# Kernel tuning notes

Measured on AMD Instinct MI355X. Metric: run time of the kernel, lower is better.

Reference implementation:

```python
import jax, jax.numpy as jnp
import numpy as np


def setup_inputs() -> dict:
    key = jax.random.key(0)
    ks = jax.random.split(key, 8)
    B, S, H, E = 4, 4096, 768, 64
    hidden_states = jax.random.normal(ks[0], (B, S, H), dtype=jnp.float32)
    attention_mask = jnp.ones((B, S), dtype=jnp.float32)
    entity_positions = jax.random.randint(ks[1], (B, E), 0, S)
    scale = 1.0 / np.sqrt(H)
    Wq = jax.random.normal(ks[2], (H, H), dtype=jnp.float32) * scale
    bq = jnp.zeros((H,), dtype=jnp.float32)
    Wk = jax.random.normal(ks[3], (H, H), dtype=jnp.float32) * scale
    bk = jnp.zeros((H,), dtype=jnp.float32)
    Wv = jax.random.normal(ks[4], (H, H), dtype=jnp.float32) * scale
    bv = jnp.zeros((H,), dtype=jnp.float32)
    return {"hidden_states": hidden_states, "attention_mask": attention_mask,
            "entity_positions": entity_positions,
            "Wq": Wq, "bq": bq, "Wk": Wk, "bk": bk, "Wv": Wv, "bv": bv}


def reference(hidden_states, attention_mask, entity_positions, Wq, bq, Wk, bk, Wv, bv):
    B, S, H = hidden_states.shape
    scaling = jnp.sqrt(jnp.asarray(H, dtype=jnp.float32))
    # Linear layers (torch: x @ W.T + b)
    q = jnp.einsum('bsh,oh->bso', hidden_states, Wq) + bq
    k = jnp.einsum('bsh,oh->bso', hidden_states, Wk) + bk
    v = jnp.einsum('bsh,oh->bso', hidden_states, Wv) + bv
    scores = jnp.einsum('bqh,bkh->bqk', q, k) / scaling  # [B,S,S]
    # Entity bias: +1.0 added to every row at each entity column (duplicates accumulate).
    # Equivalent to a per-key-column bias broadcast over query rows.
    bias_cols = jnp.zeros((B, S), dtype=scores.dtype)
    batch_idx = jnp.arange(B)[:, None]  # [B,1] broadcast against [B,E]
    bias_cols = bias_cols.at[batch_idx, entity_positions].add(1.0)
    scores = scores + bias_cols[:, None, :]
    # Attention mask over key columns.
    scores = scores + (1.0 - attention_mask)[:, None, :] * -10000.0
    probs = jax.nn.softmax(scores, axis=-1)
    context = jnp.einsum('bqk,bkh->bqh', probs, v)
    return context
```

## Files before the change

### kernel.cpp

```cpp
#include <hip/hip_runtime.h>


typedef short bf16x8 __attribute__((ext_vector_type(8)));
typedef float f32x4 __attribute__((ext_vector_type(4)));
typedef float f32x16 __attribute__((ext_vector_type(16)));

#define MFMA16(a, b, c) __builtin_amdgcn_mfma_f32_16x16x32_bf16(a, b, c, 0, 0, 0)
#define MFMA32(a, b, c) __builtin_amdgcn_mfma_f32_32x32x16_bf16(a, b, c, 0, 0, 0)

#define ASM_BAR() asm volatile("s_barrier" ::: "memory")
#define ASM_WAITV0() asm volatile("s_waitcnt vmcnt(0)" ::: "memory")
#define ASM_WAITV6() asm volatile("s_waitcnt vmcnt(6)" ::: "memory")
#define ASM_WAITL0() asm volatile("s_waitcnt lgkmcnt(0)" ::: "memory")

__device__ __forceinline__ unsigned short f2bf(float f) {
  unsigned u = __float_as_uint(f);
  u = u + 0x7FFFu + ((u >> 16) & 1u);
  return (unsigned short)(u >> 16);
}

__device__ __forceinline__ void gll16(const void* g, void* l) {
  __builtin_amdgcn_global_load_lds(
      (const __attribute__((address_space(1))) unsigned int*)g,
      (__attribute__((address_space(3))) unsigned int*)l, 16, 0, 0);
}

#define SCALE_L2E 0.05205877316f
#define LOG2E 1.4426950408889634f

__global__ void convert_w_kernel(const float* __restrict__ w0, const float* __restrict__ w1,
                                 const float* __restrict__ w2, unsigned short* __restrict__ o0,
                                 unsigned short* __restrict__ o1, unsigned short* __restrict__ o2) {
  const int which = blockIdx.y;
  const float* s = which == 0 ? w0 : (which == 1 ? w1 : w2);
  unsigned short* d = which == 0 ? o0 : (which == 1 ? o1 : o2);
  const int i = (blockIdx.x * 256 + threadIdx.x) * 4;
  float4 v = *(const float4*)(s + i);
  ushort4 r = make_ushort4(f2bf(v.x), f2bf(v.y), f2bf(v.z), f2bf(v.w));
  *(ushort4*)(d + i) = r;
}

__global__ void convert_hs_kernel(const float* __restrict__ hs, unsigned short* __restrict__ o) {
  const int i = (blockIdx.x * 256 + threadIdx.x) * 4;
  float4 v = *(const float4*)(hs + i);
  ushort4 r = make_ushort4(f2bf(v.x), f2bf(v.y), f2bf(v.z), f2bf(v.w));
  *(ushort4*)(o + i) = r;
}

__global__ void kb_init_kernel(const float* __restrict__ mask, float* __restrict__ kb) {
  const int i = blockIdx.x * 256 + threadIdx.x;
  kb[i] = (1.0f - mask[i]) * (-10000.0f * LOG2E);
}

__global__ void kb_scatter_kernel(const int* __restrict__ ep, float* __restrict__ kb) {
  const int t = threadIdx.x;
  const int b = t >> 6, e = t & 63;
  const int pos = ep[b * 64 + e];
  atomicAdd(kb + b * 4096 + pos, LOG2E);
}

__global__ __launch_bounds__(256, 3) void gemm_qk_kernel(
    const unsigned short* __restrict__ hsb, const unsigned short* __restrict__ Wqb,
    const unsigned short* __restrict__ Wkb, const float* __restrict__ bq,
    const float* __restrict__ bk, unsigned short* __restrict__ Qb,
    unsigned short* __restrict__ Kb) {
  const int z = blockIdx.z;
  const unsigned short* W = z ? Wkb : Wqb;
  const float* bias = z ? bk : bq;
  unsigned short* out = z ? Kb : Qb;
  const int m0 = blockIdx.x * 128;
  const int n0 = blockIdx.y * 128;

  __shared__ __align__(16) unsigned short Ab[2][128 * 32];
  __shared__ __align__(16) unsigned short Bb[2][128 * 32];

  const int t = threadIdx.x;
  const int lane = t & 63;
  const int w = t >> 6;
  const int wm = w & 1, wn = w >> 1;

  f32x4 acc[4][4] = {};

  auto issueT = [&](const unsigned short* src, int base, int kk, unsigned short* dst) {
#pragma unroll
    for (int r = 0; r < 2; r++) {
      int u = r * 256 + t;
      int o = u >> 2, cc = u & 3;
      int c = cc ^ ((o >> 1) & 3);
      gll16(src + (size_t)(base + o) * 768 + kk + c * 8, dst + u * 8);
    }
  };

  issueT(hsb, m0, 0, Ab[0]);
  issueT(W, n0, 0, Bb[0]);
  __syncthreads();

  for (int k = 0; k < 24; k++) {
    const int buf = k & 1;
    if (k < 23) {
      issueT(hsb, m0, (k + 1) * 32, Ab[buf ^ 1]);
      issueT(W, n0, (k + 1) * 32, Bb[buf ^ 1]);
    }
    bf16x8 af[4], bfr[4];
#pragma unroll
    for (int mt = 0; mt < 4; mt++) {
      int row = wm * 64 + mt * 16 + (lane & 15);
      int cc = (lane >> 4) ^ ((row >> 1) & 3);
      af[mt] = *(const bf16x8*)(&Ab[buf][row * 32 + cc * 8]);
    }
#pragma unroll
    for (int nt = 0; nt < 4; nt++) {
      int row = wn * 64 + nt * 16 + (lane & 15);
      int cc = (lane >> 4) ^ ((row >> 1) & 3);
      bfr[nt] = *(const bf16x8*)(&Bb[buf][row * 32 + cc * 8]);
    }
#pragma unroll
    for (int mt = 0; mt < 4; mt++)
#pragma unroll
      for (int nt = 0; nt < 4; nt++) acc[mt][nt] = MFMA16(af[mt], bfr[nt], acc[mt][nt]);
    __syncthreads();
  }

#pragma unroll
  for (int nt = 0; nt < 4; nt++) {
    int col = n0 + wn * 64 + nt * 16 + (lane & 15);
    float bv = bias[col];
#pragma unroll
    for (int mt = 0; mt < 4; mt++) {
#pragma unroll
      for (int i = 0; i < 4; i++) {
        int row = m0 + wm * 64 + mt * 16 + (lane >> 4) * 4 + i;
        out[(size_t)row * 768 + col] = f2bf(acc[mt][nt][i] + bv);
      }
    }
  }
}

__global__ __launch_bounds__(256, 3) void gemm_vt_kernel(const unsigned short* __restrict__ hsb,
                                                         const unsigned short* __restrict__ Wvb,
                                                         const float* __restrict__ bv,
                                                         unsigned short* __restrict__ Vt) {
  const int m0 = blockIdx.x * 128;
  const int n0 = blockIdx.y * 128;

  __shared__ __align__(16) unsigned short Ab[2][128 * 32];
  __shared__ __align__(16) unsigned short Bb[2][128 * 32];

  const int t = threadIdx.x;
  const int lane = t & 63;
  const int w = t >> 6;
  const int wm = w & 1, wn = w >> 1;

  f32x4 acc[4][4] = {};

  auto issueT = [&](const unsigned short* src, int base, int kk, unsigned short* dst) {
#pragma unroll
    for (int r = 0; r < 2; r++) {
      int u = r * 256 + t;
      int o = u >> 2, cc = u & 3;
      int c = cc ^ ((o >> 1) & 3);
      gll16(src + (size_t)(base + o) * 768 + kk + c * 8, dst + u * 8);
    }
  };

  issueT(Wvb, m0, 0, Ab[0]);
  issueT(hsb, n0, 0, Bb[0]);
  __syncthreads();

  for (int k = 0; k < 24; k++) {
    const int buf = k & 1;
    if (k < 23) {
      issueT(Wvb, m0, (k + 1) * 32, Ab[buf ^ 1]);
      issueT(hsb, n0, (k + 1) * 32, Bb[buf ^ 1]);
    }
    bf16x8 af[4], bfr[4];
#pragma unroll
    for (int mt = 0; mt < 4; mt++) {
      int row = wm * 64 + mt * 16 + (lane & 15);
      int cc = (lane >> 4) ^ ((row >> 1) & 3);
      af[mt] = *(const bf16x8*)(&Ab[buf][row * 32 + cc * 8]);
    }
#pragma unroll
    for (int nt = 0; nt < 4; nt++) {
      int row = wn * 64 + nt * 16 + (lane & 15);
      int cc = (lane >> 4) ^ ((row >> 1) & 3);
      bfr[nt] = *(const bf16x8*)(&Bb[buf][row * 32 + cc * 8]);
    }
#pragma unroll
    for (int mt = 0; mt < 4; mt++)
#pragma unroll
      for (int nt = 0; nt < 4; nt++) acc[mt][nt] = MFMA16(af[mt], bfr[nt], acc[mt][nt]);
    __syncthreads();
  }

#pragma unroll
  for (int mt = 0; mt < 4; mt++) {
#pragma unroll
    for (int i = 0; i < 4; i++) {
      int row_o = m0 + wm * 64 + mt * 16 + (lane >> 4) * 4 + i;
      float bb = bv[row_o];
#pragma unroll
      for (int nt = 0; nt < 4; nt++) {
        int mcol = n0 + wn * 64 + nt * 16 + (lane & 15);
        int bat = mcol >> 12, s = mcol & 4095;
        Vt[(size_t)bat * 768 * 4096 + (size_t)row_o * 4096 + s] = f2bf(acc[mt][nt][i] + bb);
      }
    }
  }
}

__global__ __launch_bounds__(512, 2) void flash_kernel(const unsigned short* __restrict__ Qb,
                                                       const unsigned short* __restrict__ Kb,
                                                       const unsigned short* __restrict__ Vt,
                                                       const float* __restrict__ KB,
                                                       float* __restrict__ out) {
  __shared__ __align__(16) unsigned short kbuf[32 * 768];
  __shared__ __align__(16) unsigned short vbuf[768 * 32];
  __shared__ __align__(16) unsigned short pbuf[4 * 64 * 8];
  __shared__ __align__(16) float sx[4 * 2 * 64 * 16];
  __shared__ __align__(16) float kb_lds[4096];
  __shared__ float st_l[64];

  const int t = threadIdx.x;
  const int lane = t & 63;
  const int w = t >> 6;
  const int rg = w & 1, hg = w >> 1;
  const int mt2 = w & 1, dg = w >> 1;
  const int flat = blockIdx.x;
  const int b = flat & 3, qt = flat >> 2;
  const int q0 = qt * 64;

  const unsigned short* Qg = Qb + (size_t)b * 4096 * 768;
  const unsigned short* Kg = Kb + (size_t)b * 4096 * 768;
  const unsigned short* Vg = Vt + (size_t)b * 768 * 4096;
  const float* KBb = KB + b * 4096;

  bf16x8 qf[12];
  {
    const unsigned short* qp =
        Qg + (size_t)(q0 + rg * 32 + (lane & 31)) * 768 + hg * 192 + (lane >> 5) * 8;
#pragma unroll
    for (int c = 0; c < 12; c++) qf[c] = *(const bf16x8*)(qp + c * 16);
  }
#pragma unroll
  for (int r = 0; r < 2; r++) {
    int i = t * 8 + r * 4;
    *(float4*)(kb_lds + i) = *(const float4*)(KBb + i);
  }

  int kidx[12];
  {
    const int key = lane & 31, l5 = lane >> 5, sw = (key >> 1) & 3;
#pragma unroll
    for (int c = 0; c < 12; c++) {
      int g = hg * 24 + c * 2 + l5;
      kidx[c] = ((g >> 2) * 128 + key * 4 + ((g & 3) ^ sw)) * 8;
    }
  }
  int vbase;
  {
    int d0 = dg * 192 + (lane & 15);
    vbase = (d0 * 4 + ((lane >> 4) ^ ((d0 >> 1) & 3))) * 8;
  }
  int pidx0, pidx1;
  {
    int g2 = lane >> 4;
    int r0 = mt2 * 32 + (lane & 15);
    pidx0 = (g2 * 64 + (r0 ^ (g2 * 2))) * 8;
    pidx1 = (g2 * 64 + ((r0 + 16) ^ (g2 * 2))) * 8;
  }
  const int s_rg = t >> 8, s_q = (t >> 6) & 3, s_l = t & 63;
  const int col = s_l & 31;
  const int row_b = s_rg * 32 + 8 * s_q + 4 * (s_l >> 5);
  int pslot[4];
#pragma unroll
  for (int jj = 0; jj < 4; jj++)
    pslot[jj] = ((col >> 3) * 64 + ((row_b + jj) ^ ((col >> 3) * 2))) * 8 + (col & 7);
  float* sxw = sx + hg * 2048 + (rg * 64 + lane) * 16;
  const int wswz = (lane >> 1) & 3;
  const float* sxr = sx + (s_rg * 64 + s_l) * 16 + (s_q ^ ((s_l >> 1) & 3)) * 4;

  f32x4 oacc[24] = {};
  float racc0 = 0.0f, racc1 = 0.0f, racc2 = 0.0f, racc3 = 0.0f;

  auto issueK = [&](int j) {
#pragma unroll
    for (int r = 0; r < 6; r++) {
      int u = r * 512 + t;
      int ks = u >> 7, rem = u & 127, key = rem >> 2, cs = rem & 3;
      int c = cs ^ ((key >> 1) & 3);
      gll16(Kg + (size_t)(j * 32 + key) * 768 + ks * 32 + c * 8, &kbuf[u * 8]);
    }
  };
  auto issueV = [&](int j) {
#pragma unroll
    for (int r = 0; r < 6; r++) {
      int u = r * 512 + t;
      int d = u >> 2, cs = u & 3;
      int c = cs ^ ((d >> 1) & 3);
      gll16(Vg + (size_t)d * 4096 + j * 32 + c * 8, &vbuf[u * 8]);
    }
  };

  issueK(0);
  ASM_WAITV0();
  ASM_BAR();

  for (int j = 0; j < 128; j++) {
    issueV(j);
    f32x16 s = {};
#pragma unroll
    for (int c = 0; c < 12; c++) {
      bf16x8 kf = *(const bf16x8*)(kbuf + kidx[c]);
      s = MFMA32(qf[c], kf, s);
    }
#pragma unroll
    for (int i = 0; i < 4; i++) {
      *(float4*)(sxw + (i ^ wswz) * 4) =
          make_float4(s[i * 4], s[i * 4 + 1], s[i * 4 + 2], s[i * 4 + 3]);
    }
    ASM_WAITL0();
    ASM_BAR();
    if (j < 127) issueK(j + 1);
    {
      float4 a0 = *(const float4*)(sxr);
      float4 a1 = *(const float4*)(sxr + 2048);
      float4 a2 = *(const float4*)(sxr + 4096);
      float4 a3 = *(const float4*)(sxr + 6144);
      float kbias = kb_lds[j * 32 + col];
      float e0 = __builtin_amdgcn_exp2f(fmaf(a0.x + a1.x + a2.x + a3.x, SCALE_L2E, kbias));
      float e1 = __builtin_amdgcn_exp2f(fmaf(a0.y + a1.y + a2.y + a3.y, SCALE_L2E, kbias));
      float e2 = __builtin_amdgcn_exp2f(fmaf(a0.z + a1.z + a2.z + a3.z, SCALE_L2E, kbias));
      float e3 = __builtin_amdgcn_exp2f(fmaf(a0.w + a1.w + a2.w + a3.w, SCALE_L2E, kbias));
      pbuf[pslot[0]] = f2bf(e0);
      pbuf[pslot[1]] = f2bf(e1);
      pbuf[pslot[2]] = f2bf(e2);
      pbuf[pslot[3]] = f2bf(e3);
      racc0 += e0;
      racc1 += e1;
      racc2 += e2;
      racc3 += e3;
    }
    ASM_WAITL0();
    if (j < 127) {
      ASM_WAITV6();
    } else {
      ASM_WAITV0();
    }
    ASM_BAR();
    {
      bf16x8 pf0 = *(const bf16x8*)(pbuf + pidx0);
      bf16x8 pf1 = *(const bf16x8*)(pbuf + pidx1);
#pragma unroll
      for (int dt = 0; dt < 12; dt++) {
        bf16x8 vf = *(const bf16x8*)(vbuf + vbase + dt * 512);
        oacc[dt] = MFMA16(pf0, vf, oacc[dt]);
        oacc[12 + dt] = MFMA16(pf1, vf, oacc[12 + dt]);
      }
    }
    ASM_WAITV0();
    ASM_BAR();
  }
#pragma unroll
  for (int m = 1; m < 32; m <<= 1) {
    racc0 += __shfl_xor(racc0, m, 32);
    racc1 += __shfl_xor(racc1, m, 32);
    racc2 += __shfl_xor(racc2, m, 32);
    racc3 += __shfl_xor(racc3, m, 32);
  }
  if ((s_l & 31) == 0) {
    st_l[row_b] = racc0;
    st_l[row_b + 1] = racc1;
    st_l[row_b + 2] = racc2;
    st_l[row_b + 3] = racc3;
  }
  __syncthreads();
#pragma unroll
  for (int pt = 0; pt < 2; pt++) {
    int rb = mt2 * 32 + pt * 16 + (lane >> 4) * 4;
    float l0 = 1.0f / st_l[rb], l1 = 1.0f / st_l[rb + 1];
    float l2 = 1.0f / st_l[rb + 2], l3 = 1.0f / st_l[rb + 3];
#pragma unroll
    for (int dt = 0; dt < 12; dt++) {
      int d = dg * 192 + dt * 16 + (lane & 15);
      size_t base = ((size_t)(b * 4096 + q0 + rb)) * 768 + d;
      out[base] = oacc[pt * 12 + dt][0] * l0;
      out[base + 768] = oacc[pt * 12 + dt][1] * l1;
      out[base + 2 * 768] = oacc[pt * 12 + dt][2] * l2;
      out[base + 3 * 768] = oacc[pt * 12 + dt][3] * l3;
    }
  }
}

extern "C" void kernel_launch(void* const* d_in, const int* in_sizes, int n_in, void* d_out,
                              int out_size, void* d_ws, size_t ws_size, hipStream_t stream) {
  const float* hs = (const float*)d_in[0];
  const float* mask = (const float*)d_in[1];
  const int* ep = (const int*)d_in[2];
  const float* Wq = (const float*)d_in[3];
  const float* bq = (const float*)d_in[4];
  const float* Wk = (const float*)d_in[5];
  const float* bk = (const float*)d_in[6];
  const float* Wv = (const float*)d_in[7];
  const float* bv = (const float*)d_in[8];
  float* outp = (float*)d_out;

  char* ws = (char*)d_ws;
  unsigned short* Qb = (unsigned short*)(ws);
  unsigned short* Kb = (unsigned short*)(ws + 25165824);
  unsigned short* Vt = (unsigned short*)(ws + 50331648);
  unsigned short* Wqb = (unsigned short*)(ws + 75497472);
  unsigned short* Wkb = (unsigned short*)(ws + 76677120);
  unsigned short* Wvb = (unsigned short*)(ws + 77856768);
  float* KBp = (float*)(ws + 79036416);
  unsigned short* Hsb = (unsigned short*)(ws + 79101952);

  convert_w_kernel<<<dim3(576, 3), 256, 0, stream>>>(Wq, Wk, Wv, Wqb, Wkb, Wvb);
  convert_hs_kernel<<<12288, 256, 0, stream>>>(hs, Hsb);
  kb_init_kernel<<<64, 256, 0, stream>>>(mask, KBp);
  kb_scatter_kernel<<<1, 256, 0, stream>>>(ep, KBp);
  gemm_qk_kernel<<<dim3(128, 6, 2), 256, 0, stream>>>(Hsb, Wqb, Wkb, bq, bk, Qb, Kb);
  gemm_vt_kernel<<<dim3(6, 128), 256, 0, stream>>>(Hsb, Wvb, bv, Vt);
  flash_kernel<<<256, 512, 0, stream>>>(Qb, Kb, Vt, KBp, outp);
}
```

Measured before the change: 485.3 us.

## Triple-buffer QKV projection GEMMs with prefetch distance two and partial vmcnt waits

```diff
diff --git a/kernel.cpp b/kernel.cpp
--- a/kernel.cpp
+++ b/kernel.cpp
@@ -10,6 +10,7 @@
 
 #define ASM_BAR() asm volatile("s_barrier" ::: "memory")
 #define ASM_WAITV0() asm volatile("s_waitcnt vmcnt(0)" ::: "memory")
+#define ASM_WAITV4() asm volatile("s_waitcnt vmcnt(4)" ::: "memory")
 #define ASM_WAITV6() asm volatile("s_waitcnt vmcnt(6)" ::: "memory")
 #define ASM_WAITL0() asm volatile("s_waitcnt lgkmcnt(0)" ::: "memory")
 
@@ -71,8 +72,8 @@
   const int m0 = blockIdx.x * 128;
   const int n0 = blockIdx.y * 128;
 
-  __shared__ __align__(16) unsigned short Ab[2][128 * 32];
-  __shared__ __align__(16) unsigned short Bb[2][128 * 32];
+  __shared__ __align__(16) unsigned short Ab[3][128 * 32];
+  __shared__ __align__(16) unsigned short Bb[3][128 * 32];
 
   const int t = threadIdx.x;
   const int lane = t & 63;
@@ -93,13 +94,17 @@
 
   issueT(hsb, m0, 0, Ab[0]);
   issueT(W, n0, 0, Bb[0]);
-  __syncthreads();
+  issueT(hsb, m0, 32, Ab[1]);
+  issueT(W, n0, 32, Bb[1]);
+  ASM_WAITV4();
+  ASM_BAR();
 
   for (int k = 0; k < 24; k++) {
-    const int buf = k & 1;
-    if (k < 23) {
-      issueT(hsb, m0, (k + 1) * 32, Ab[buf ^ 1]);
-      issueT(W, n0, (k + 1) * 32, Bb[buf ^ 1]);
+    const int buf = k % 3;
+    if (k < 22) {
+      const int nb = (k + 2) % 3;
+      issueT(hsb, m0, (k + 2) * 32, Ab[nb]);
+      issueT(W, n0, (k + 2) * 32, Bb[nb]);
     }
     bf16x8 af[4], bfr[4];
 #pragma unroll
@@ -118,7 +123,12 @@
     for (int mt = 0; mt < 4; mt++)
 #pragma unroll
       for (int nt = 0; nt < 4; nt++) acc[mt][nt] = MFMA16(af[mt], bfr[nt], acc[mt][nt]);
-    __syncthreads();
+    if (k < 22) {
+      ASM_WAITV4();
+    } else {
+      ASM_WAITV0();
+    }
+    ASM_BAR();
   }
 
 #pragma unroll
@@ -143,8 +153,8 @@
   const int m0 = blockIdx.x * 128;
   const int n0 = blockIdx.y * 128;
 
-  __shared__ __align__(16) unsigned short Ab[2][128 * 32];
-  __shared__ __align__(16) unsigned short Bb[2][128 * 32];
+  __shared__ __align__(16) unsigned short Ab[3][128 * 32];
+  __shared__ __align__(16) unsigned short Bb[3][128 * 32];
 
   const int t = threadIdx.x;
   const int lane = t & 63;
@@ -165,13 +175,17 @@
 
   issueT(Wvb, m0, 0, Ab[0]);
   issueT(hsb, n0, 0, Bb[0]);
-  __syncthreads();
+  issueT(Wvb, m0, 32, Ab[1]);
+  issueT(hsb, n0, 32, Bb[1]);
+  ASM_WAITV4();
+  ASM_BAR();
 
   for (int k = 0; k < 24; k++) {
-    const int buf = k & 1;
-    if (k < 23) {
-      issueT(Wvb, m0, (k + 1) * 32, Ab[buf ^ 1]);
-      issueT(hsb, n0, (k + 1) * 32, Bb[buf ^ 1]);
+    const int buf = k % 3;
+    if (k < 22) {
+      const int nb = (k + 2) % 3;
+      issueT(Wvb, m0, (k + 2) * 32, Ab[nb]);
+      issueT(hsb, n0, (k + 2) * 32, Bb[nb]);
     }
     bf16x8 af[4], bfr[4];
 #pragma unroll
@@ -190,7 +204,12 @@
     for (int mt = 0; mt < 4; mt++)
 #pragma unroll
       for (int nt = 0; nt < 4; nt++) acc[mt][nt] = MFMA16(af[mt], bfr[nt], acc[mt][nt]);
-    __syncthreads();
+    if (k < 22) {
+      ASM_WAITV4();
+    } else {
+      ASM_WAITV0();
+    }
+    ASM_BAR();
   }
 
 #pragma unroll
```

New measurement: 484.0 us. No clear change (-0.3%).
